# Kernel optimization log

Hardware: AMD Instinct MI355X
Metric: run time of the kernel (lower is better)

Reference implementation:

```python
import jax, jax.numpy as jnp
import numpy as np

B, T, C, H = 4, 2048, 1024, 16
D = C // H
SCALE = D ** -0.5


def setup_inputs() -> dict:
    key = jax.random.key(0)
    ks = jax.random.split(key, 5)
    x = jax.random.normal(ks[0], (B, T, C), dtype=jnp.float32)
    key_padding_mask = jnp.zeros((B, T), dtype=bool)  # True = masked key
    W_qkv = jax.random.normal(ks[1], (C, 3 * C), dtype=jnp.float32) * (C ** -0.5)
    b_qkv = jax.random.normal(ks[2], (3 * C,), dtype=jnp.float32) * 0.02
    W_proj = jax.random.normal(ks[3], (C, C), dtype=jnp.float32) * (C ** -0.5)
    b_proj = jax.random.normal(ks[4], (C,), dtype=jnp.float32) * 0.02
    return {"x": x, "key_padding_mask": key_padding_mask, "W_qkv": W_qkv,
            "b_qkv": b_qkv, "W_proj": W_proj, "b_proj": b_proj}


def reference(x, key_padding_mask, W_qkv, b_qkv, W_proj, b_proj):
    Bx, Tx, Cx = x.shape
    qkv = x @ W_qkv + b_qkv                      # [B,T,3C]
    qkv = qkv.reshape(Bx, Tx, 3, H, D)
    q = jnp.transpose(qkv[:, :, 0], (0, 2, 1, 3))  # [B,H,T,D]
    k = jnp.transpose(qkv[:, :, 1], (0, 2, 1, 3))
    v = jnp.transpose(qkv[:, :, 2], (0, 2, 1, 3))
    attn = jnp.einsum('bhqd,bhkd->bhqk', q, k) * SCALE  # [B,H,T,T]
    causal = jnp.triu(jnp.ones((Tx, Tx), dtype=bool), k=1)  # True = masked
    neg_inf = jnp.finfo(attn.dtype).min
    attn = jnp.where(causal[None, None, :, :], neg_inf, attn)
    attn = jnp.where(key_padding_mask[:, None, None, :], neg_inf, attn)
    attn = jax.nn.softmax(attn, axis=-1)
    out = jnp.einsum('bhqk,bhkd->bhqd', attn, v)  # [B,H,T,D]
    out = jnp.transpose(out, (0, 2, 1, 3)).reshape(Bx, Tx, Cx)
    return out @ W_proj + b_proj
```

## Files before the change

kernel.cpp:

```cpp
#include <hip/hip_runtime.h>


typedef __bf16 bf16;
typedef __bf16 bf16x4 __attribute__((ext_vector_type(4)));
typedef __bf16 bf16x8 __attribute__((ext_vector_type(8)));
typedef float f32x4 __attribute__((ext_vector_type(4)));

#define MFMA(a, b, c) __builtin_amdgcn_mfma_f32_16x16x32_bf16((a), (b), (c), 0, 0, 0)

typedef const __attribute__((address_space(1))) void* gas_ptr;
typedef __attribute__((address_space(3))) void* las_ptr;

__device__ __forceinline__ void gload_lds16(const bf16* g, bf16* lds) {
  __builtin_amdgcn_global_load_lds((gas_ptr)g, (las_ptr)lds, 16, 0, 0);
}

__global__ __launch_bounds__(256) void k_cvt(const float* __restrict__ src,
                                             bf16* __restrict__ dst, int n4) {
  int i = blockIdx.x * 256 + threadIdx.x;
  if (i >= n4) return;
  float4 v = ((const float4*)src)[i];
  bf16x4 o = { (bf16)v.x, (bf16)v.y, (bf16)v.z, (bf16)v.w };
  ((bf16x4*)dst)[i] = o;
}

__global__ __launch_bounds__(256) void k_transpose(const float* __restrict__ src,
                                                   bf16* __restrict__ dst,
                                                   int R, int C) {
  __shared__ float tile[32][33];
  int c0 = blockIdx.x * 32, r0 = blockIdx.y * 32;
  int x = threadIdx.x & 31, y = threadIdx.x >> 5;
#pragma unroll
  for (int i = 0; i < 4; ++i)
    tile[y + i * 8][x] = src[(size_t)(r0 + y + i * 8) * C + (c0 + x)];
  __syncthreads();
#pragma unroll
  for (int i = 0; i < 4; ++i)
    dst[(size_t)(c0 + y + i * 8) * R + (r0 + x)] = (bf16)tile[x][y + i * 8];
}

__global__ void k_maskflags(const unsigned char* __restrict__ kpm,
                            int* __restrict__ flags) {
  int i = threadIdx.x;
  const uint4* p = (const uint4*)(kpm + i * 128);
  unsigned acc = 0;
#pragma unroll
  for (int j = 0; j < 8; ++j) { uint4 v = p[j]; acc |= v.x | v.y | v.z | v.w; }
  flags[i] = (acc != 0) ? 1 : 0;
}

template <int EPI>
__global__ __launch_bounds__(256, 2)
void k_gemm_bt(const bf16* __restrict__ A, const bf16* __restrict__ Bt,
               const float* __restrict__ bias, float* __restrict__ fout,
               bf16* __restrict__ qp, bf16* __restrict__ kp,
               bf16* __restrict__ vtp, int M, int N, int K) {
  __shared__ bf16 Ab[2][128 * 32];
  __shared__ bf16 Bb[2][128 * 32];
  const int tid = threadIdx.x;
  const int wave = tid >> 6, lane = tid & 63;
  const int m0 = blockIdx.x * 128, n0 = blockIdx.y * 128;
  const int wr = wave >> 1, wc = wave & 1;
  const int lrow = lane & 15, kb = (lane >> 4) * 8;
  f32x4 acc[4][4] = {};
  const int nkt = K >> 5;

  auto stage = [&](int buf, int kt) {
#pragma unroll
    for (int i = 0; i < 2; ++i) {
      int c = i * 4 + wave;
      const bf16* ga = A + (size_t)(m0 + c * 16 + (lane >> 2)) * K + kt * 32 + (lane & 3) * 8;
      gload_lds16(ga, &Ab[buf][c * 512]);
      const bf16* gb = Bt + (size_t)(n0 + c * 16 + (lane >> 2)) * K + kt * 32 + (lane & 3) * 8;
      gload_lds16(gb, &Bb[buf][c * 512]);
    }
  };

  stage(0, 0);
  asm volatile("s_waitcnt vmcnt(0)" ::: "memory");
  __syncthreads();
  int cur = 0;
  for (int kt = 0; kt < nkt; ++kt) {
    if (kt + 1 < nkt) stage(cur ^ 1, kt + 1);
    bf16x8 af[4], bfr[4];
#pragma unroll
    for (int m = 0; m < 4; ++m)
      af[m] = *(const bf16x8*)&Ab[cur][(wr * 64 + m * 16 + lrow) * 32 + kb];
#pragma unroll
    for (int n = 0; n < 4; ++n)
      bfr[n] = *(const bf16x8*)&Bb[cur][(wc * 64 + n * 16 + lrow) * 32 + kb];
#pragma unroll
    for (int m = 0; m < 4; ++m)
#pragma unroll
      for (int n = 0; n < 4; ++n)
        acc[m][n] = MFMA(af[m], bfr[n], acc[m][n]);
    asm volatile("s_waitcnt vmcnt(0)" ::: "memory");
    __syncthreads();
    cur ^= 1;
  }

#pragma unroll
  for (int m = 0; m < 4; ++m) {
#pragma unroll
    for (int n = 0; n < 4; ++n) {
      const int col = n0 + wc * 64 + n * 16 + lrow;
      const int row0 = m0 + wr * 64 + m * 16 + (lane >> 4) * 4;
      const float bv = bias[col];
      if (EPI == 0) {
        const int which = col >> 10;
        const int h = (col >> 6) & 15, d = col & 63;
        const int b = row0 >> 11, t0 = row0 & 2047;
        const int bh = b * 16 + h;
        if (which == 2) {
          bf16x4 pk;
#pragma unroll
          for (int j = 0; j < 4; ++j) pk[j] = (bf16)(acc[m][n][j] + bv);
          *(bf16x4*)&vtp[((size_t)bh * 64 + d) * 2048 + t0] = pk;
        } else {
          bf16* dstp = (which == 0) ? qp : kp;
          const float sc = (which == 0) ? 0.18033688011112042f : 1.0f;
#pragma unroll
          for (int j = 0; j < 4; ++j)
            dstp[((size_t)bh * 2048 + (t0 + j)) * 64 + d] = (bf16)((acc[m][n][j] + bv) * sc);
        }
      } else {
#pragma unroll
        for (int j = 0; j < 4; ++j)
          fout[(size_t)(row0 + j) * N + col] = acc[m][n][j] + bv;
      }
    }
  }
}

__global__ __launch_bounds__(256, 3)
void k_flash(const bf16* __restrict__ Q, const bf16* __restrict__ Kg,
             const bf16* __restrict__ Vt, const unsigned char* __restrict__ kpm,
             const int* __restrict__ tflags, bf16* __restrict__ O) {
  const int bh = blockIdx.x;
  const int b = bh >> 4, h = bh & 15;
  const int qt = 15 - (int)blockIdx.y;
  const int tid = threadIdx.x, wave = tid >> 6, lane = tid & 63;
  const int lrow = lane & 15, g = lane >> 4;

  __shared__ bf16 Kt[128 * 64];
  __shared__ bf16 Vts[64 * 128];
  __shared__ bf16 PT[4][2048];

  const bf16* Kbh = Kg + (size_t)bh * 2048 * 64;
  const bf16* Vbh = Vt + (size_t)bh * 64 * 2048;

  const int k_src_col = (((lane & 7) ^ (lane >> 3)) << 3);
  const int rowc = lane >> 3;
  const int ptb2 = g * 256 + lrow * 8;

  const bf16* Qbase = Q + ((size_t)bh * 2048 + qt * 128 + wave * 32) * 64;
  bf16x8 qf[2][2];
#pragma unroll
  for (int m = 0; m < 2; ++m)
#pragma unroll
    for (int ks = 0; ks < 2; ++ks)
      qf[m][ks] = *(const bf16x8*)&Qbase[(m * 16 + lrow) * 64 + ks * 32 + g * 8];

  f32x4 oacc[2][4] = {};
  float rl[2][4] = {};

  for (int kvt = 0; kvt <= qt; ++kvt) {
#pragma unroll
    for (int i = 0; i < 4; ++i) {
      int c = i * 4 + wave;
      gload_lds16(Kbh + (size_t)(kvt * 128 + c * 8 + rowc) * 64 + k_src_col, &Kt[c * 512]);
    }
#pragma unroll
    for (int i = 0; i < 4; ++i) {
      int c = i * 4 + wave;
      int vs = (((lane & 15) ^ (((c & 1) << 2) | g)) << 3);
      gload_lds16(Vbh + (size_t)(c * 4 + g) * 2048 + kvt * 128 + vs, &Vts[c * 512]);
    }
    asm volatile("s_waitcnt vmcnt(0)" ::: "memory");
    __builtin_amdgcn_s_barrier();
    __builtin_amdgcn_sched_barrier(0);

    f32x4 s[2][8];
    __builtin_amdgcn_s_setprio(1);
#pragma unroll
    for (int n = 0; n < 8; ++n) {
      const int row = n * 16 + lrow;
      bf16x8 kf0 = *(const bf16x8*)&Kt[row * 64 + ((g ^ (lrow & 7)) << 3)];
      bf16x8 kf1 = *(const bf16x8*)&Kt[row * 64 + (((4 + g) ^ (lrow & 7)) << 3)];
#pragma unroll
      for (int m = 0; m < 2; ++m) {
        f32x4 t = {};
        t = MFMA(qf[m][0], kf0, t);
        t = MFMA(qf[m][1], kf1, t);
        s[m][n] = t;
      }
    }
    __builtin_amdgcn_s_setprio(0);

    if (tflags[b * 16 + kvt]) {
#pragma unroll
      for (int n = 0; n < 8; ++n) {
        const int col = kvt * 128 + n * 16 + lrow;
        if (kpm[b * 2048 + col]) {
#pragma unroll
          for (int m = 0; m < 2; ++m)
#pragma unroll
            for (int j = 0; j < 4; ++j) s[m][n][j] = -1e30f;
        }
      }
    }
    if (kvt == qt) {
#pragma unroll
      for (int n = 0; n < 8; ++n) {
        const int ccol = n * 16 + lrow;
#pragma unroll
        for (int m = 0; m < 2; ++m)
#pragma unroll
          for (int j = 0; j < 4; ++j) {
            const int crow = wave * 32 + m * 16 + g * 4 + j;
            if (ccol > crow) s[m][n][j] = -1e30f;
          }
      }
    }

#pragma unroll
    for (int m = 0; m < 2; ++m) {
#pragma unroll
      for (int n = 0; n < 8; ++n) {
        bf16x4 pk;
#pragma unroll
        for (int j = 0; j < 4; ++j) {
          const float p = exp2f(s[m][n][j]);
          rl[m][j] += p;
          pk[j] = (bf16)p;
        }
        const int woff = (n * 16 + lrow) * 32 + g * 8;
        *(bf16x4*)((char*)&PT[wave][0] + woff) = pk;
      }
      asm volatile("s_waitcnt lgkmcnt(0)" ::: "memory");
      __builtin_amdgcn_sched_barrier(0);
#pragma unroll
      for (int ks = 0; ks < 4; ++ks) {
        bf16x4 plo, phi;
        las_ptr pa_ = (las_ptr)((char*)&PT[wave][0] + ptb2);
        asm volatile("ds_read_b64_tr_b16 %0, %1 offset:%2"
                     : "=v"(plo) : "v"(pa_), "i"(ks * 1024));
        asm volatile("ds_read_b64_tr_b16 %0, %1 offset:%2"
                     : "=v"(phi) : "v"(pa_), "i"(ks * 1024 + 128));
        bf16x8 vf[4];
#pragma unroll
        for (int nt = 0; nt < 4; ++nt) {
          const int d = nt * 16 + lrow;
          vf[nt] = *(const bf16x8*)((const char*)Vts + d * 256 +
                                    (((ks * 4 + g) ^ (lrow & 7)) << 4));
        }
        asm volatile("s_waitcnt lgkmcnt(0)" ::: "memory");
        __builtin_amdgcn_sched_barrier(0);
        bf16x8 pa = __builtin_shufflevector(plo, phi, 0, 1, 2, 3, 4, 5, 6, 7);
        __builtin_amdgcn_s_setprio(1);
#pragma unroll
        for (int nt = 0; nt < 4; ++nt)
          oacc[m][nt] = MFMA(pa, vf[nt], oacc[m][nt]);
        __builtin_amdgcn_s_setprio(0);
      }
    }

    __builtin_amdgcn_s_barrier();
    __builtin_amdgcn_sched_barrier(0);
  }

#pragma unroll
  for (int off = 1; off < 16; off <<= 1)
#pragma unroll
    for (int m = 0; m < 2; ++m)
#pragma unroll
      for (int j = 0; j < 4; ++j) rl[m][j] += __shfl_xor(rl[m][j], off, 64);

#pragma unroll
  for (int m = 0; m < 2; ++m)
#pragma unroll
    for (int nt = 0; nt < 4; ++nt)
#pragma unroll
      for (int j = 0; j < 4; ++j) {
        const int t = qt * 128 + wave * 32 + m * 16 + g * 4 + j;
        const int c = h * 64 + nt * 16 + lrow;
        O[((size_t)b * 2048 + t) * 1024 + c] = (bf16)(oacc[m][nt][j] / rl[m][j]);
      }
}

extern "C" void kernel_launch(void* const* d_in, const int* in_sizes, int n_in,
                              void* d_out, int out_size, void* d_ws, size_t ws_size,
                              hipStream_t stream) {
  const float* x = (const float*)d_in[0];
  const unsigned char* kpm = (const unsigned char*)d_in[1];
  const float* Wqkv = (const float*)d_in[2];
  const float* bqkv = (const float*)d_in[3];
  const float* Wproj = (const float*)d_in[4];
  const float* bproj = (const float*)d_in[5];
  float* out = (float*)d_out;
  char* ws = (char*)d_ws;

  bf16* xb     = (bf16*)(ws + 0);
  bf16* WqkvT  = (bf16*)(ws + 16777216);
  bf16* WprojT = (bf16*)(ws + 23068672);
  bf16* Qb     = (bf16*)(ws + 25165824);
  bf16* Kb     = (bf16*)(ws + 41943040);
  bf16* Vtb    = (bf16*)(ws + 58720256);
  bf16* AOb    = (bf16*)(ws + 75497472);
  int*  tflags = (int*)(ws + 0);

  k_cvt<<<8192, 256, 0, stream>>>(x, xb, 2097152);
  k_transpose<<<dim3(96, 32), 256, 0, stream>>>(Wqkv, WqkvT, 1024, 3072);
  k_transpose<<<dim3(32, 32), 256, 0, stream>>>(Wproj, WprojT, 1024, 1024);
  k_gemm_bt<0><<<dim3(64, 24), 256, 0, stream>>>(xb, WqkvT, bqkv, nullptr, Qb, Kb,
                                                 Vtb, 8192, 3072, 1024);
  k_maskflags<<<1, 64, 0, stream>>>(kpm, tflags);
  k_flash<<<dim3(64, 16), 256, 0, stream>>>(Qb, Kb, Vtb, kpm, tflags, AOb);
  k_gemm_bt<1><<<dim3(64, 8), 256, 0, stream>>>(AOb, WprojT, bproj, out, nullptr,
                                                nullptr, nullptr, 8192, 1024, 1024);
}
```

Before: 185.7 us.

## Skip masked diagonal blocks, store K/V in fragment order, compute row sums via MFMA

On the diagonal KV tile, each wave now skips QK^T column blocks and PV k-steps that lie entirely above its causal boundary. K and V tiles are loaded into LDS already in MFMA fragment order, so each fragment read is a contiguous per-lane 16-byte load with no XOR swizzle arithmetic. The softmax denominator now comes from an extra MFMA against a ones vector on the bf16-rounded probabilities, replacing the per-element float adds and the final cross-lane shuffle reduction. The linear fragment layout may add LDS bank conflicts, and the skipped paths add wave-dependent branches inside unrolled loops.

```diff
diff --git a/kernel.cpp b/kernel.cpp
--- a/kernel.cpp
+++ b/kernel.cpp
@@ -142,15 +142,13 @@
   const int tid = threadIdx.x, wave = tid >> 6, lane = tid & 63;
   const int lrow = lane & 15, g = lane >> 4;
 
-  __shared__ bf16 Kt[128 * 64];
-  __shared__ bf16 Vts[64 * 128];
+  __shared__ bf16 Kt[16 * 512];
+  __shared__ bf16 Vts[16 * 512];
   __shared__ bf16 PT[4][2048];
 
   const bf16* Kbh = Kg + (size_t)bh * 2048 * 64;
   const bf16* Vbh = Vt + (size_t)bh * 64 * 2048;
 
-  const int k_src_col = (((lane & 7) ^ (lane >> 3)) << 3);
-  const int rowc = lane >> 3;
   const int ptb2 = g * 256 + lrow * 8;
 
   const bf16* Qbase = Q + ((size_t)bh * 2048 + qt * 128 + wave * 32) * 64;
@@ -161,38 +159,47 @@
     for (int ks = 0; ks < 2; ++ks)
       qf[m][ks] = *(const bf16x8*)&Qbase[(m * 16 + lrow) * 64 + ks * 32 + g * 8];
 
+  const bf16 one_bf = (bf16)1.0f;
+  const bf16x8 ones8 = { one_bf, one_bf, one_bf, one_bf, one_bf, one_bf, one_bf, one_bf };
+
   f32x4 oacc[2][4] = {};
-  float rl[2][4] = {};
+  f32x4 osum[2] = {};
 
   for (int kvt = 0; kvt <= qt; ++kvt) {
 #pragma unroll
     for (int i = 0; i < 4; ++i) {
       int c = i * 4 + wave;
-      gload_lds16(Kbh + (size_t)(kvt * 128 + c * 8 + rowc) * 64 + k_src_col, &Kt[c * 512]);
+      gload_lds16(Kbh + (size_t)(kvt * 128 + (c >> 1) * 16 + lrow) * 64 + (c & 1) * 32 + g * 8,
+                  &Kt[c * 512]);
     }
 #pragma unroll
     for (int i = 0; i < 4; ++i) {
       int c = i * 4 + wave;
-      int vs = (((lane & 15) ^ (((c & 1) << 2) | g)) << 3);
-      gload_lds16(Vbh + (size_t)(c * 4 + g) * 2048 + kvt * 128 + vs, &Vts[c * 512]);
+      gload_lds16(Vbh + (size_t)((c & 3) * 16 + lrow) * 2048 + kvt * 128 + (c >> 2) * 32 + g * 8,
+                  &Vts[c * 512]);
     }
     asm volatile("s_waitcnt vmcnt(0)" ::: "memory");
     __builtin_amdgcn_s_barrier();
     __builtin_amdgcn_sched_barrier(0);
 
+    const bool diag = (kvt == qt);
+    const int nmax = diag ? (2 * wave + 2) : 8;
+    const int ksmax = diag ? (wave + 1) : 4;
+
     f32x4 s[2][8];
     __builtin_amdgcn_s_setprio(1);
 #pragma unroll
     for (int n = 0; n < 8; ++n) {
-      const int row = n * 16 + lrow;
-      bf16x8 kf0 = *(const bf16x8*)&Kt[row * 64 + ((g ^ (lrow & 7)) << 3)];
-      bf16x8 kf1 = *(const bf16x8*)&Kt[row * 64 + (((4 + g) ^ (lrow & 7)) << 3)];
-#pragma unroll
-      for (int m = 0; m < 2; ++m) {
-        f32x4 t = {};
-        t = MFMA(qf[m][0], kf0, t);
-        t = MFMA(qf[m][1], kf1, t);
-        s[m][n] = t;
+      if (n < nmax) {
+        bf16x8 kf0 = *(const bf16x8*)&Kt[(n * 2 + 0) * 512 + lane * 8];
+        bf16x8 kf1 = *(const bf16x8*)&Kt[(n * 2 + 1) * 512 + lane * 8];
+#pragma unroll
+        for (int m = 0; m < 2; ++m) {
+          f32x4 t = {};
+          t = MFMA(qf[m][0], kf0, t);
+          t = MFMA(qf[m][1], kf1, t);
+          s[m][n] = t;
+        }
       }
     }
     __builtin_amdgcn_s_setprio(0);
@@ -200,68 +207,70 @@
     if (tflags[b * 16 + kvt]) {
 #pragma unroll
       for (int n = 0; n < 8; ++n) {
-        const int col = kvt * 128 + n * 16 + lrow;
-        if (kpm[b * 2048 + col]) {
+        if (n < nmax) {
+          const int col = kvt * 128 + n * 16 + lrow;
+          if (kpm[b * 2048 + col]) {
+#pragma unroll
+            for (int m = 0; m < 2; ++m)
+#pragma unroll
+              for (int j = 0; j < 4; ++j) s[m][n][j] = -1e30f;
+          }
+        }
+      }
+    }
+    if (diag) {
+#pragma unroll
+      for (int n = 0; n < 8; ++n) {
+        if (n < nmax) {
+          const int ccol = n * 16 + lrow;
 #pragma unroll
           for (int m = 0; m < 2; ++m)
 #pragma unroll
-            for (int j = 0; j < 4; ++j) s[m][n][j] = -1e30f;
-        }
-      }
-    }
-    if (kvt == qt) {
+            for (int j = 0; j < 4; ++j) {
+              const int crow = wave * 32 + m * 16 + g * 4 + j;
+              if (ccol > crow) s[m][n][j] = -1e30f;
+            }
+        }
+      }
+    }
+
+#pragma unroll
+    for (int m = 0; m < 2; ++m) {
 #pragma unroll
       for (int n = 0; n < 8; ++n) {
-        const int ccol = n * 16 + lrow;
-#pragma unroll
-        for (int m = 0; m < 2; ++m)
-#pragma unroll
-          for (int j = 0; j < 4; ++j) {
-            const int crow = wave * 32 + m * 16 + g * 4 + j;
-            if (ccol > crow) s[m][n][j] = -1e30f;
-          }
-      }
-    }
-
-#pragma unroll
-    for (int m = 0; m < 2; ++m) {
-#pragma unroll
-      for (int n = 0; n < 8; ++n) {
-        bf16x4 pk;
-#pragma unroll
-        for (int j = 0; j < 4; ++j) {
-          const float p = exp2f(s[m][n][j]);
-          rl[m][j] += p;
-          pk[j] = (bf16)p;
-        }
-        const int woff = (n * 16 + lrow) * 32 + g * 8;
-        *(bf16x4*)((char*)&PT[wave][0] + woff) = pk;
+        if (n < nmax) {
+          bf16x4 pk;
+#pragma unroll
+          for (int j = 0; j < 4; ++j) pk[j] = (bf16)exp2f(s[m][n][j]);
+          const int woff = (n * 16 + lrow) * 32 + g * 8;
+          *(bf16x4*)((char*)&PT[wave][0] + woff) = pk;
+        }
       }
       asm volatile("s_waitcnt lgkmcnt(0)" ::: "memory");
       __builtin_amdgcn_sched_barrier(0);
 #pragma unroll
       for (int ks = 0; ks < 4; ++ks) {
-        bf16x4 plo, phi;
-        las_ptr pa_ = (las_ptr)((char*)&PT[wave][0] + ptb2);
-        asm volatile("ds_read_b64_tr_b16 %0, %1 offset:%2"
-                     : "=v"(plo) : "v"(pa_), "i"(ks * 1024));
-        asm volatile("ds_read_b64_tr_b16 %0, %1 offset:%2"
-                     : "=v"(phi) : "v"(pa_), "i"(ks * 1024 + 128));
-        bf16x8 vf[4];
-#pragma unroll
-        for (int nt = 0; nt < 4; ++nt) {
-          const int d = nt * 16 + lrow;
-          vf[nt] = *(const bf16x8*)((const char*)Vts + d * 256 +
-                                    (((ks * 4 + g) ^ (lrow & 7)) << 4));
-        }
-        asm volatile("s_waitcnt lgkmcnt(0)" ::: "memory");
-        __builtin_amdgcn_sched_barrier(0);
-        bf16x8 pa = __builtin_shufflevector(plo, phi, 0, 1, 2, 3, 4, 5, 6, 7);
-        __builtin_amdgcn_s_setprio(1);
-#pragma unroll
-        for (int nt = 0; nt < 4; ++nt)
-          oacc[m][nt] = MFMA(pa, vf[nt], oacc[m][nt]);
-        __builtin_amdgcn_s_setprio(0);
+        if (ks < ksmax) {
+          bf16x4 plo, phi;
+          las_ptr pa_ = (las_ptr)((char*)&PT[wave][0] + ptb2);
+          asm volatile("ds_read_b64_tr_b16 %0, %1 offset:%2"
+                       : "=v"(plo) : "v"(pa_), "i"(ks * 1024));
+          asm volatile("ds_read_b64_tr_b16 %0, %1 offset:%2"
+                       : "=v"(phi) : "v"(pa_), "i"(ks * 1024 + 128));
+          bf16x8 vf[4];
+#pragma unroll
+          for (int nt = 0; nt < 4; ++nt)
+            vf[nt] = *(const bf16x8*)&Vts[(ks * 4 + nt) * 512 + lane * 8];
+          asm volatile("s_waitcnt lgkmcnt(0)" ::: "memory");
+          __builtin_amdgcn_sched_barrier(0);
+          bf16x8 pa = __builtin_shufflevector(plo, phi, 0, 1, 2, 3, 4, 5, 6, 7);
+          __builtin_amdgcn_s_setprio(1);
+#pragma unroll
+          for (int nt = 0; nt < 4; ++nt)
+            oacc[m][nt] = MFMA(pa, vf[nt], oacc[m][nt]);
+          osum[m] = MFMA(pa, ones8, osum[m]);
+          __builtin_amdgcn_s_setprio(0);
+        }
       }
     }
 
@@ -270,13 +279,6 @@
   }
 
 #pragma unroll
-  for (int off = 1; off < 16; off <<= 1)
-#pragma unroll
-    for (int m = 0; m < 2; ++m)
-#pragma unroll
-      for (int j = 0; j < 4; ++j) rl[m][j] += __shfl_xor(rl[m][j], off, 64);
-
-#pragma unroll
   for (int m = 0; m < 2; ++m)
 #pragma unroll
     for (int nt = 0; nt < 4; ++nt)
@@ -284,7 +286,7 @@
       for (int j = 0; j < 4; ++j) {
         const int t = qt * 128 + wave * 32 + m * 16 + g * 4 + j;
         const int c = h * 64 + nt * 16 + lrow;
-        O[((size_t)b * 2048 + t) * 1024 + c] = (bf16)(oacc[m][nt][j] / rl[m][j]);
+        O[((size_t)b * 2048 + t) * 1024 + c] = (bf16)(oacc[m][nt][j] / osum[m][j]);
       }
 }
 
```

Result: no change. 187.2 us (+0.8%).
